# Optimization experiments

Hardware: AMD Instinct MI355X
Metric: run time of the kernel (lower is better)

The kernel has to match this reference:

```python
import jax, jax.numpy as jnp
import numpy as np

# Episode configuration (matches init_kwargs); feature map fixed by module: [64,7,7]
N_WAY, K_SHOT, Q_QUERY, PRJ = 10, 5, 100, 16
DIM, H, W = 64, 7, 7
N_SUP = N_WAY * K_SHOT * PRJ      # 800 support samples
N_QRY = N_WAY * Q_QUERY * PRJ     # 16000 query samples
B = N_SUP + N_QRY                 # 16800
TRIU_I, TRIU_J = np.triu_indices(DIM)  # row-major upper-tri indices, matches torch nonzero order


def setup_inputs() -> dict:
    key = jax.random.key(0)
    k1, k2 = jax.random.split(key)
    feat = jax.random.normal(k1, (B, DIM, H, W), dtype=jnp.float32)
    label = jax.random.randint(k2, (N_QRY,), 0, N_WAY, dtype=jnp.int64)
    # nn.Parameter init: log(1/(2*h*w)) * ones(1,1)
    temp = jnp.log(jnp.ones((1, 1), dtype=jnp.float32) / (2.0 * H * W))
    return {"feat": feat, "temp": temp, "label": label}


def _bdcovpool(x, t):
    # x: [B, dim, h, w] -> Brownian distance covariance matrix [B, dim, dim]
    b, d, h, w = x.shape
    xm = x.reshape(b, d, h * w)
    g = jnp.einsum('bim,bjm->bij', xm, xm)            # x @ x^T, [B,d,d]
    dg = jnp.diagonal(g, axis1=1, axis2=2)            # [B,d]
    # I_M @ (G*I) + (G*I) @ I_M - 2G  ==  diag_j + diag_i - 2G
    dcov = dg[:, None, :] + dg[:, :, None] - 2.0 * g
    dcov = jnp.sqrt(jnp.exp(t) * jnp.clip(dcov, 0.0) + 1e-5)
    # double centering: dcov - rowmean - colmean + totalmean
    rm = jnp.mean(dcov, axis=2, keepdims=True)        # (1/d) dcov @ I_M
    cm = jnp.mean(dcov, axis=1, keepdims=True)        # (1/d) I_M @ dcov
    tm = jnp.mean(dcov, axis=(1, 2), keepdims=True)   # (1/d^2) I_M @ dcov @ I_M
    return dcov - rm - cm + tm


def reference(feat, temp, label):
    v = _bdcovpool(feat, temp)                        # [B, 64, 64]
    tv = v[:, TRIU_I, TRIU_J]                         # Triuvec: [B, 2080]
    support = tv[:N_SUP].reshape(N_WAY, K_SHOT * PRJ, -1).mean(axis=1)  # [n_way, 2080]
    query = tv[N_SUP:]                                # [N_QRY, 2080]
    # negative squared euclidean distance (expanded form of sum((x-y)^2))
    q2 = jnp.sum(query * query, axis=1, keepdims=True)          # [N_QRY,1]
    s2 = jnp.sum(support * support, axis=1)[None, :]             # [1,n_way]
    score = -(q2 + s2 - 2.0 * jnp.einsum('nd,md->nm', query, support))  # [N_QRY, n_way]
    logp = jax.nn.log_softmax(score, axis=-1)
    loss = -jnp.mean(jnp.take_along_axis(logp, label[:, None], axis=1))
    return score, loss
```

## Files before the change

kernel.cpp:

```cpp
#include <hip/hip_runtime.h>
#include <math.h>

#define NWAY   10
#define DIMD   64
#define HWN    49
#define NSUP   800
#define NQRY   16000
#define NTRI   2080
#define FEAT_PER (DIMD*HWN)
#define LDST   68
#define KPAD   72
#define STP    12

typedef __attribute__((ext_vector_type(8))) short bf16x8;
typedef __attribute__((ext_vector_type(4))) float f32x4;

struct __align__(16) BDCShared {
    union {
        float dcov[DIMD*LDST];
        unsigned short hl[2*DIMD*KPAD];
    } u;
    float dg[DIMD];
    float rm[DIMD];
    float w4[4];
    float red[4*12];
};

__device__ __forceinline__ void k2ij(int k, int& io, int& jo) {
    int ii = (int)floorf((129.0f - sqrtf(16641.0f - 8.0f*(float)k)) * 0.5f);
    int off = ii*(129-ii)/2;
    if (off > k) { --ii; off = ii*(129-ii)/2; }
    else {
        int off2 = (ii+1)*(128-ii)/2;
        if (off2 <= k) { ii += 1; off = off2; }
    }
    io = ii;
    jo = ii + (k - off);
}

__device__ __forceinline__ unsigned cvt_pk_bf16(float a, float b) {
    unsigned r;
    asm("v_cvt_pk_bf16_f32 %0, %1, %2" : "=v"(r) : "v"(a), "v"(b));
    return r;
}

__device__ __forceinline__ float bdc_compute(const float* __restrict__ feat,
                                             float et, int sample,
                                             BDCShared& sm) {
    const int tid = threadIdx.x;
    unsigned short* Hh = sm.u.hl;
    unsigned short* Lh = sm.u.hl + DIMD*KPAD;

    {
        const int d = tid & 63, hq = tid >> 6;
        const float* rowp = feat + (size_t)sample * FEAT_PER + d*HWN + hq*16;
        float x[16];
        if (hq < 3) {
            #pragma unroll
            for (int i = 0; i < 16; ++i) x[i] = rowp[i];
        } else {
            x[0] = rowp[0];
            #pragma unroll
            for (int i = 1; i < 16; ++i) x[i] = 0.0f;
        }
        unsigned hp[8], lp[8];
        #pragma unroll
        for (int i = 0; i < 8; ++i) {
            unsigned h = cvt_pk_bf16(x[2*i], x[2*i+1]);
            float h0 = __uint_as_float(h << 16);
            float h1 = __uint_as_float(h & 0xffff0000u);
            hp[i] = h;
            lp[i] = cvt_pk_bf16(x[2*i] - h0, x[2*i+1] - h1);
        }
        uint4* hd = (uint4*)&Hh[d*KPAD + hq*16];
        uint4* ld = (uint4*)&Lh[d*KPAD + hq*16];
        hd[0] = make_uint4(hp[0], hp[1], hp[2], hp[3]);
        hd[1] = make_uint4(hp[4], hp[5], hp[6], hp[7]);
        ld[0] = make_uint4(lp[0], lp[1], lp[2], lp[3]);
        ld[1] = make_uint4(lp[4], lp[5], lp[6], lp[7]);
    }
    __syncthreads();

    const int wv = tid >> 6, lane = tid & 63;
    const int qd = lane >> 4, c15 = lane & 15;
    const int abase = (16*wv + c15)*KPAD + qd*8;
    bf16x8 AH0 = *(const bf16x8*)&Hh[abase];
    bf16x8 AH1 = *(const bf16x8*)&Hh[abase + 32];
    bf16x8 AL0 = *(const bf16x8*)&Lh[abase];
    bf16x8 AL1 = *(const bf16x8*)&Lh[abase + 32];

    f32x4 acc[4];
    #pragma unroll
    for (int J = 0; J < 4; ++J) {
        const int bbase = (16*J + c15)*KPAD + qd*8;
        bf16x8 BH0 = *(const bf16x8*)&Hh[bbase];
        bf16x8 BH1 = *(const bf16x8*)&Hh[bbase + 32];
        bf16x8 BL0 = *(const bf16x8*)&Lh[bbase];
        bf16x8 BL1 = *(const bf16x8*)&Lh[bbase + 32];
        f32x4 a = {0.f, 0.f, 0.f, 0.f};
        a = __builtin_amdgcn_mfma_f32_16x16x32_bf16(AH0, BH0, a, 0, 0, 0);
        a = __builtin_amdgcn_mfma_f32_16x16x32_bf16(AH1, BH1, a, 0, 0, 0);
        a = __builtin_amdgcn_mfma_f32_16x16x32_bf16(AL0, BH0, a, 0, 0, 0);
        a = __builtin_amdgcn_mfma_f32_16x16x32_bf16(AL1, BH1, a, 0, 0, 0);
        a = __builtin_amdgcn_mfma_f32_16x16x32_bf16(AH0, BL0, a, 0, 0, 0);
        a = __builtin_amdgcn_mfma_f32_16x16x32_bf16(AH1, BL1, a, 0, 0, 0);
        acc[J] = a;
    }

    #pragma unroll
    for (int J = 0; J < 4; ++J) {
        if (J == wv) {
            #pragma unroll
            for (int r = 0; r < 4; ++r)
                if (c15 == 4*qd + r) sm.dg[16*wv + c15] = acc[J][r];
        }
    }
    __syncthreads();

    float* dcov = sm.u.dcov;
    f32x4 dgi = *(const f32x4*)&sm.dg[16*wv + 4*qd];
    float rs0 = 0.f, rs1 = 0.f, rs2 = 0.f, rs3 = 0.f;
    #pragma unroll
    for (int J = 0; J < 4; ++J) {
        float dgj = sm.dg[16*J + c15];
        f32x4 o;
        #pragma unroll
        for (int r = 0; r < 4; ++r) {
            float t2 = fmaf(-2.0f, acc[J][r], dgi[r] + dgj);
            t2 = fmaxf(t2, 0.0f);
            o[r] = __builtin_amdgcn_sqrtf(fmaf(et, t2, 1e-5f));
        }
        rs0 += o[0]; rs1 += o[1]; rs2 += o[2]; rs3 += o[3];
        *(f32x4*)&dcov[(16*J + c15)*LDST + 16*wv + 4*qd] = o;
    }
    #pragma unroll
    for (int o = 1; o < 16; o <<= 1) {
        rs0 += __shfl_xor(rs0, o, 64);
        rs1 += __shfl_xor(rs1, o, 64);
        rs2 += __shfl_xor(rs2, o, 64);
        rs3 += __shfl_xor(rs3, o, 64);
    }
    if (c15 == 0) {
        f32x4 rmv = {rs0*(1.0f/64.0f), rs1*(1.0f/64.0f),
                     rs2*(1.0f/64.0f), rs3*(1.0f/64.0f)};
        *(f32x4*)&sm.rm[16*wv + 4*qd] = rmv;
    }
    float tt = (rs0 + rs1) + (rs2 + rs3);
    tt += __shfl_xor(tt, 16, 64);
    tt += __shfl_xor(tt, 32, 64);
    if (lane == 0) sm.w4[wv] = tt;
    __syncthreads();
    return (sm.w4[0] + sm.w4[1] + sm.w4[2] + sm.w4[3]) * (1.0f/4096.0f);
}

__global__ void kern_init(unsigned* __restrict__ table,
                          float* __restrict__ s2,
                          float* __restrict__ loss_slot) {
    int i = blockIdx.x * 256 + threadIdx.x;
    if (i < NTRI) {
        int ii, jj; k2ij(i, ii, jj);
        table[i] = ((unsigned)(ii*LDST + jj) << 16) | ((unsigned)ii << 8) | (unsigned)jj;
    }
    if (i < NWAY) s2[i] = 0.0f;
    if (i == 0) loss_slot[0] = 0.0f;
}

__global__ __launch_bounds__(256, 6) void kern_support(const float* __restrict__ feat,
                                                       const float* __restrict__ temp,
                                                       const unsigned* __restrict__ table,
                                                       float* __restrict__ tvout) {
    __shared__ BDCShared sm;
    float et = __expf(temp[0]);
    int s = blockIdx.x;
    float tm = bdc_compute(feat, et, s, sm);
    float* dst = tvout + (size_t)s * NTRI;
    for (int k = threadIdx.x; k < NTRI; k += 256) {
        unsigned t = table[k];
        dst[k] = sm.u.dcov[t >> 16] - sm.rm[(t >> 8) & 63] - sm.rm[t & 63] + tm;
    }
}

__global__ __launch_bounds__(256) void kern_reduce(const float* __restrict__ tv,
                                                   float* __restrict__ supT,
                                                   float* __restrict__ s2) {
    __shared__ float red[4];
    int m = blockIdx.x / 9, kc = blockIdx.x % 9;
    int k = kc*256 + threadIdx.x;
    float S = 0.0f;
    if (k < NTRI) {
        const float* p = tv + (size_t)(80*m) * NTRI + k;
        float a0 = 0.f, a1 = 0.f, a2 = 0.f, a3 = 0.f;
        for (int s4 = 0; s4 < 80; s4 += 4) {
            a0 += p[(size_t)(s4+0)*NTRI];
            a1 += p[(size_t)(s4+1)*NTRI];
            a2 += p[(size_t)(s4+2)*NTRI];
            a3 += p[(size_t)(s4+3)*NTRI];
        }
        S = ((a0+a1)+(a2+a3)) * (1.0f/80.0f);
        supT[k*STP + m] = S;
    }
    float ps = S * S;
    int lane = threadIdx.x & 63, wv = threadIdx.x >> 6;
    #pragma unroll
    for (int o = 32; o > 0; o >>= 1) ps += __shfl_xor(ps, o, 64);
    if (lane == 0) red[wv] = ps;
    __syncthreads();
    if (threadIdx.x == 0) atomicAdd(&s2[m], red[0]+red[1]+red[2]+red[3]);
}

__global__ __launch_bounds__(256, 6) void kern_query(const float* __restrict__ feat,
                                                     const float* __restrict__ temp,
                                                     const unsigned* __restrict__ table,
                                                     const float* __restrict__ supT,
                                                     const float* __restrict__ s2,
                                                     float* __restrict__ out) {
    __shared__ BDCShared sm;
    float et = __expf(temp[0]);
    int qn = blockIdx.x;
    float tm = bdc_compute(feat, et, NSUP + qn, sm);

    float qq = 0.0f;
    float cr[NWAY];
    #pragma unroll
    for (int m = 0; m < NWAY; ++m) cr[m] = 0.0f;

    for (int k = threadIdx.x; k < NTRI; k += 256) {
        unsigned t = table[k];
        float v = sm.u.dcov[t >> 16] - sm.rm[(t >> 8) & 63] - sm.rm[t & 63] + tm;
        qq = fmaf(v, v, qq);
        const float4* sp = (const float4*)(supT + (size_t)k * STP);
        float4 sa = sp[0], sb = sp[1], sc = sp[2];
        cr[0] = fmaf(v, sa.x, cr[0]);
        cr[1] = fmaf(v, sa.y, cr[1]);
        cr[2] = fmaf(v, sa.z, cr[2]);
        cr[3] = fmaf(v, sa.w, cr[3]);
        cr[4] = fmaf(v, sb.x, cr[4]);
        cr[5] = fmaf(v, sb.y, cr[5]);
        cr[6] = fmaf(v, sb.z, cr[6]);
        cr[7] = fmaf(v, sb.w, cr[7]);
        cr[8] = fmaf(v, sc.x, cr[8]);
        cr[9] = fmaf(v, sc.y, cr[9]);
    }

    int lane = threadIdx.x & 63, wv = threadIdx.x >> 6;
    #pragma unroll
    for (int m = 0; m < NWAY; ++m) {
        float v = cr[m];
        #pragma unroll
        for (int o = 32; o > 0; o >>= 1) v += __shfl_xor(v, o, 64);
        cr[m] = v;
    }
    #pragma unroll
    for (int o = 32; o > 0; o >>= 1) qq += __shfl_xor(qq, o, 64);
    if (lane == 0) {
        #pragma unroll
        for (int m = 0; m < NWAY; ++m) sm.red[wv*12 + m] = cr[m];
        sm.red[wv*12 + 10] = qq;
    }
    __syncthreads();
    if (threadIdx.x < NWAY) {
        int m = threadIdx.x;
        float CR = sm.red[m] + sm.red[12+m] + sm.red[24+m] + sm.red[36+m];
        float QQ = sm.red[10] + sm.red[22] + sm.red[34] + sm.red[46];
        out[(size_t)qn * NWAY + m] = -(QQ + s2[m] - 2.0f*CR);
    }
}

__global__ __launch_bounds__(256) void kern_loss(const float* __restrict__ score,
                                                 const int* __restrict__ label,
                                                 float* __restrict__ loss_out) {
    __shared__ float red[4];
    int n = blockIdx.x * 256 + threadIdx.x;
    float lsum = 0.0f;
    if (n < NQRY) {
        const float* srow = score + (size_t)n * NWAY;
        float s[NWAY];
        float mx = -1e30f;
        #pragma unroll
        for (int m = 0; m < NWAY; ++m) { s[m] = srow[m]; mx = fmaxf(mx, s[m]); }
        float se = 0.0f;
        #pragma unroll
        for (int m = 0; m < NWAY; ++m) se += __expf(s[m] - mx);
        float lse = mx + __logf(se);
        lsum = lse - s[label[n]];
    }
    int lane = threadIdx.x & 63, wv = threadIdx.x >> 6;
    #pragma unroll
    for (int o = 32; o > 0; o >>= 1) lsum += __shfl_xor(lsum, o, 64);
    if (lane == 0) red[wv] = lsum;
    __syncthreads();
    if (threadIdx.x == 0)
        atomicAdd(loss_out, (red[0] + red[1] + red[2] + red[3]) * (1.0f / (float)NQRY));
}

extern "C" void kernel_launch(void* const* d_in, const int* in_sizes, int n_in,
                              void* d_out, int out_size, void* d_ws, size_t ws_size,
                              hipStream_t stream) {
    const float* feat = (const float*)d_in[0];
    const float* temp = (const float*)d_in[1];
    const int*   label = (const int*)d_in[2];
    float* out = (float*)d_out;

    float*    tv    = (float*)d_ws;
    float*    supT  = tv + (size_t)NSUP * NTRI;
    float*    s2    = supT + NTRI*STP;
    unsigned* table = (unsigned*)(s2 + 16);
    float* loss_slot = out + (size_t)NQRY * NWAY;

    kern_init<<<(NTRI + 255)/256, 256, 0, stream>>>(table, s2, loss_slot);
    kern_support<<<NSUP, 256, 0, stream>>>(feat, temp, table, tv);
    kern_reduce<<<NWAY*9, 256, 0, stream>>>(tv, supT, s2);
    kern_query<<<NQRY, 256, 0, stream>>>(feat, temp, table, supT, s2, out);
    kern_loss<<<(NQRY + 255)/256, 256, 0, stream>>>(out, label, loss_slot);
}
```

Before: 346.6 us.

## Keep dcov in registers and score queries against symmetric full support matrices

```diff
diff --git a/kernel.cpp b/kernel.cpp
--- a/kernel.cpp
+++ b/kernel.cpp
@@ -8,22 +8,20 @@
 #define NQRY   16000
 #define NTRI   2080
 #define FEAT_PER (DIMD*HWN)
-#define LDST   68
 #define KPAD   72
-#define STP    12
 
 typedef __attribute__((ext_vector_type(8))) short bf16x8;
 typedef __attribute__((ext_vector_type(4))) float f32x4;
 
 struct __align__(16) BDCShared {
     union {
-        float dcov[DIMD*LDST];
         unsigned short hl[2*DIMD*KPAD];
+        float part[256*12];
     } u;
     float dg[DIMD];
     float rm[DIMD];
     float w4[4];
-    float red[4*12];
+    float red[16];
 };
 
 __device__ __forceinline__ void k2ij(int k, int& io, int& jo) {
@@ -46,7 +44,7 @@
 
 __device__ __forceinline__ float bdc_compute(const float* __restrict__ feat,
                                              float et, int sample,
-                                             BDCShared& sm) {
+                                             BDCShared& sm, f32x4* o, f32x4& rmi) {
     const int tid = threadIdx.x;
     unsigned short* Hh = sm.u.hl;
     unsigned short* Lh = sm.u.hl + DIMD*KPAD;
@@ -117,28 +115,25 @@
     }
     __syncthreads();
 
-    float* dcov = sm.u.dcov;
     f32x4 dgi = *(const f32x4*)&sm.dg[16*wv + 4*qd];
     float rs0 = 0.f, rs1 = 0.f, rs2 = 0.f, rs3 = 0.f;
     #pragma unroll
     for (int J = 0; J < 4; ++J) {
         float dgj = sm.dg[16*J + c15];
-        f32x4 o;
         #pragma unroll
         for (int r = 0; r < 4; ++r) {
             float t2 = fmaf(-2.0f, acc[J][r], dgi[r] + dgj);
             t2 = fmaxf(t2, 0.0f);
-            o[r] = __builtin_amdgcn_sqrtf(fmaf(et, t2, 1e-5f));
-        }
-        rs0 += o[0]; rs1 += o[1]; rs2 += o[2]; rs3 += o[3];
-        *(f32x4*)&dcov[(16*J + c15)*LDST + 16*wv + 4*qd] = o;
-    }
-    #pragma unroll
-    for (int o = 1; o < 16; o <<= 1) {
-        rs0 += __shfl_xor(rs0, o, 64);
-        rs1 += __shfl_xor(rs1, o, 64);
-        rs2 += __shfl_xor(rs2, o, 64);
-        rs3 += __shfl_xor(rs3, o, 64);
+            o[J][r] = __builtin_amdgcn_sqrtf(fmaf(et, t2, 1e-5f));
+        }
+        rs0 += o[J][0]; rs1 += o[J][1]; rs2 += o[J][2]; rs3 += o[J][3];
+    }
+    #pragma unroll
+    for (int off = 1; off < 16; off <<= 1) {
+        rs0 += __shfl_xor(rs0, off, 64);
+        rs1 += __shfl_xor(rs1, off, 64);
+        rs2 += __shfl_xor(rs2, off, 64);
+        rs3 += __shfl_xor(rs3, off, 64);
     }
     if (c15 == 0) {
         f32x4 rmv = {rs0*(1.0f/64.0f), rs1*(1.0f/64.0f),
@@ -150,6 +145,10 @@
     tt += __shfl_xor(tt, 32, 64);
     if (lane == 0) sm.w4[wv] = tt;
     __syncthreads();
+    rmi[0] = rs0 * (1.0f/64.0f);
+    rmi[1] = rs1 * (1.0f/64.0f);
+    rmi[2] = rs2 * (1.0f/64.0f);
+    rmi[3] = rs3 * (1.0f/64.0f);
     return (sm.w4[0] + sm.w4[1] + sm.w4[2] + sm.w4[3]) * (1.0f/4096.0f);
 }
 
@@ -159,7 +158,7 @@
     int i = blockIdx.x * 256 + threadIdx.x;
     if (i < NTRI) {
         int ii, jj; k2ij(i, ii, jj);
-        table[i] = ((unsigned)(ii*LDST + jj) << 16) | ((unsigned)ii << 8) | (unsigned)jj;
+        table[i] = ((unsigned)ii << 8) | (unsigned)jj;
     }
     if (i < NWAY) s2[i] = 0.0f;
     if (i == 0) loss_slot[0] = 0.0f;
@@ -167,26 +166,41 @@
 
 __global__ __launch_bounds__(256, 6) void kern_support(const float* __restrict__ feat,
                                                        const float* __restrict__ temp,
-                                                       const unsigned* __restrict__ table,
                                                        float* __restrict__ tvout) {
     __shared__ BDCShared sm;
     float et = __expf(temp[0]);
     int s = blockIdx.x;
-    float tm = bdc_compute(feat, et, s, sm);
+    f32x4 o[4]; f32x4 rmi;
+    float tm = bdc_compute(feat, et, s, sm, o, rmi);
+
+    const int tid = threadIdx.x;
+    const int wv = tid >> 6, lane = tid & 63;
+    const int qd = lane >> 4, c15 = lane & 15;
+    const int iB = 16*wv + 4*qd;
     float* dst = tvout + (size_t)s * NTRI;
-    for (int k = threadIdx.x; k < NTRI; k += 256) {
-        unsigned t = table[k];
-        dst[k] = sm.u.dcov[t >> 16] - sm.rm[(t >> 8) & 63] - sm.rm[t & 63] + tm;
+    #pragma unroll
+    for (int J = 0; J < 4; ++J) {
+        int j = 16*J + c15;
+        float rmj = sm.rm[j];
+        #pragma unroll
+        for (int r = 0; r < 4; ++r) {
+            int i = iB + r;
+            if (j >= i) {
+                float v = o[J][r] - rmi[r] - rmj + tm;
+                dst[i*(129 - i)/2 + (j - i)] = v;
+            }
+        }
     }
 }
 
 __global__ __launch_bounds__(256) void kern_reduce(const float* __restrict__ tv,
-                                                   float* __restrict__ supT,
+                                                   const unsigned* __restrict__ table,
+                                                   float* __restrict__ Sfull,
                                                    float* __restrict__ s2) {
     __shared__ float red[4];
     int m = blockIdx.x / 9, kc = blockIdx.x % 9;
     int k = kc*256 + threadIdx.x;
-    float S = 0.0f;
+    float ps = 0.0f;
     if (k < NTRI) {
         const float* p = tv + (size_t)(80*m) * NTRI + k;
         float a0 = 0.f, a1 = 0.f, a2 = 0.f, a3 = 0.f;
@@ -196,13 +210,17 @@
             a2 += p[(size_t)(s4+2)*NTRI];
             a3 += p[(size_t)(s4+3)*NTRI];
         }
-        S = ((a0+a1)+(a2+a3)) * (1.0f/80.0f);
-        supT[k*STP + m] = S;
-    }
-    float ps = S * S;
+        float S = ((a0+a1)+(a2+a3)) * (1.0f/80.0f);
+        unsigned t = table[k];
+        int ii = (int)(t >> 8), jj = (int)(t & 255u);
+        float* Sm = Sfull + (size_t)m * 4096;
+        Sm[ii*64 + jj] = S;
+        Sm[jj*64 + ii] = S;
+        ps = S * S;
+    }
     int lane = threadIdx.x & 63, wv = threadIdx.x >> 6;
     #pragma unroll
-    for (int o = 32; o > 0; o >>= 1) ps += __shfl_xor(ps, o, 64);
+    for (int off = 32; off > 0; off >>= 1) ps += __shfl_xor(ps, off, 64);
     if (lane == 0) red[wv] = ps;
     __syncthreads();
     if (threadIdx.x == 0) atomicAdd(&s2[m], red[0]+red[1]+red[2]+red[3]);
@@ -210,60 +228,82 @@
 
 __global__ __launch_bounds__(256, 6) void kern_query(const float* __restrict__ feat,
                                                      const float* __restrict__ temp,
-                                                     const unsigned* __restrict__ table,
-                                                     const float* __restrict__ supT,
+                                                     const float* __restrict__ Sfull,
                                                      const float* __restrict__ s2,
                                                      float* __restrict__ out) {
     __shared__ BDCShared sm;
     float et = __expf(temp[0]);
     int qn = blockIdx.x;
-    float tm = bdc_compute(feat, et, NSUP + qn, sm);
-
-    float qq = 0.0f;
+    f32x4 o[4]; f32x4 rmi;
+    float tm = bdc_compute(feat, et, NSUP + qn, sm, o, rmi);
+
+    const int tid = threadIdx.x;
+    const int wv = tid >> 6, lane = tid & 63;
+    const int qd = lane >> 4, c15 = lane & 15;
+    const int iB = 16*wv + 4*qd;
+
+    f32x4 u[4];
+    #pragma unroll
+    for (int J = 0; J < 4; ++J) {
+        float rmj = sm.rm[16*J + c15];
+        #pragma unroll
+        for (int r = 0; r < 4; ++r) {
+            float v = o[J][r] - rmi[r] - rmj + tm;
+            u[J][r] = 0.5f * v;
+        }
+    }
+    float dadj = 0.0f;
+    if ((c15 >> 2) == qd) {
+        int r0 = c15 & 3;
+        float ud = u[wv][r0] * 2.0f;
+        u[wv][r0] = ud;
+        dadj = ud * ud;
+    }
+    float qq2 = 0.0f;
+    #pragma unroll
+    for (int J = 0; J < 4; ++J) {
+        #pragma unroll
+        for (int r = 0; r < 4; ++r) qq2 = fmaf(u[J][r], u[J][r], qq2);
+    }
+    float qq = 2.0f*qq2 - dadj;
+
     float cr[NWAY];
     #pragma unroll
     for (int m = 0; m < NWAY; ++m) cr[m] = 0.0f;
-
-    for (int k = threadIdx.x; k < NTRI; k += 256) {
-        unsigned t = table[k];
-        float v = sm.u.dcov[t >> 16] - sm.rm[(t >> 8) & 63] - sm.rm[t & 63] + tm;
-        qq = fmaf(v, v, qq);
-        const float4* sp = (const float4*)(supT + (size_t)k * STP);
-        float4 sa = sp[0], sb = sp[1], sc = sp[2];
-        cr[0] = fmaf(v, sa.x, cr[0]);
-        cr[1] = fmaf(v, sa.y, cr[1]);
-        cr[2] = fmaf(v, sa.z, cr[2]);
-        cr[3] = fmaf(v, sa.w, cr[3]);
-        cr[4] = fmaf(v, sb.x, cr[4]);
-        cr[5] = fmaf(v, sb.y, cr[5]);
-        cr[6] = fmaf(v, sb.z, cr[6]);
-        cr[7] = fmaf(v, sb.w, cr[7]);
-        cr[8] = fmaf(v, sc.x, cr[8]);
-        cr[9] = fmaf(v, sc.y, cr[9]);
-    }
-
-    int lane = threadIdx.x & 63, wv = threadIdx.x >> 6;
-    #pragma unroll
-    for (int m = 0; m < NWAY; ++m) {
-        float v = cr[m];
-        #pragma unroll
-        for (int o = 32; o > 0; o >>= 1) v += __shfl_xor(v, o, 64);
-        cr[m] = v;
-    }
-    #pragma unroll
-    for (int o = 32; o > 0; o >>= 1) qq += __shfl_xor(qq, o, 64);
-    if (lane == 0) {
-        #pragma unroll
-        for (int m = 0; m < NWAY; ++m) sm.red[wv*12 + m] = cr[m];
-        sm.red[wv*12 + 10] = qq;
-    }
-    __syncthreads();
-    if (threadIdx.x < NWAY) {
-        int m = threadIdx.x;
-        float CR = sm.red[m] + sm.red[12+m] + sm.red[24+m] + sm.red[36+m];
-        float QQ = sm.red[10] + sm.red[22] + sm.red[34] + sm.red[46];
-        out[(size_t)qn * NWAY + m] = -(QQ + s2[m] - 2.0f*CR);
-    }
+    #pragma unroll
+    for (int J = 0; J < 4; ++J) {
+        const float* sp = Sfull + (16*J + c15)*64 + iB;
+        f32x4 uj = u[J];
+        #pragma unroll
+        for (int m = 0; m < NWAY; ++m) {
+            f32x4 sf = *(const f32x4*)(sp + (size_t)m*4096);
+            cr[m] = fmaf(uj[0], sf[0], cr[m]);
+            cr[m] = fmaf(uj[1], sf[1], cr[m]);
+            cr[m] = fmaf(uj[2], sf[2], cr[m]);
+            cr[m] = fmaf(uj[3], sf[3], cr[m]);
+        }
+    }
+
+    float* part = sm.u.part;
+    f32x4 p0 = {cr[0], cr[1], cr[2], cr[3]};
+    f32x4 p1 = {cr[4], cr[5], cr[6], cr[7]};
+    f32x4 p2 = {cr[8], cr[9], qq, 0.0f};
+    *(f32x4*)&part[tid*12 + 0] = p0;
+    *(f32x4*)&part[tid*12 + 4] = p1;
+    *(f32x4*)&part[tid*12 + 8] = p2;
+    __syncthreads();
+    if (tid < 176) {
+        int m = tid >> 4, g = tid & 15;
+        float s = 0.0f;
+        #pragma unroll
+        for (int t = 0; t < 16; ++t) s += part[(g + 16*t)*12 + m];
+        #pragma unroll
+        for (int off = 1; off < 16; off <<= 1) s += __shfl_xor(s, off, 64);
+        if (g == 0) sm.red[m] = s;
+    }
+    __syncthreads();
+    if (tid < NWAY)
+        out[(size_t)qn * NWAY + tid] = -(sm.red[10] + s2[tid] - 2.0f*sm.red[tid]);
 }
 
 __global__ __launch_bounds__(256) void kern_loss(const float* __restrict__ score,
@@ -286,7 +326,7 @@
     }
     int lane = threadIdx.x & 63, wv = threadIdx.x >> 6;
     #pragma unroll
-    for (int o = 32; o > 0; o >>= 1) lsum += __shfl_xor(lsum, o, 64);
+    for (int off = 32; off > 0; off >>= 1) lsum += __shfl_xor(lsum, off, 64);
     if (lane == 0) red[wv] = lsum;
     __syncthreads();
     if (threadIdx.x == 0)
@@ -296,20 +336,21 @@
 extern "C" void kernel_launch(void* const* d_in, const int* in_sizes, int n_in,
                               void* d_out, int out_size, void* d_ws, size_t ws_size,
                               hipStream_t stream) {
+    (void)in_sizes; (void)n_in; (void)out_size; (void)ws_size;
     const float* feat = (const float*)d_in[0];
     const float* temp = (const float*)d_in[1];
     const int*   label = (const int*)d_in[2];
     float* out = (float*)d_out;
 
     float*    tv    = (float*)d_ws;
-    float*    supT  = tv + (size_t)NSUP * NTRI;
-    float*    s2    = supT + NTRI*STP;
+    float*    Sfull = tv + (size_t)NSUP * NTRI;
+    float*    s2    = Sfull + (size_t)NWAY * 4096;
     unsigned* table = (unsigned*)(s2 + 16);
     float* loss_slot = out + (size_t)NQRY * NWAY;
 
     kern_init<<<(NTRI + 255)/256, 256, 0, stream>>>(table, s2, loss_slot);
-    kern_support<<<NSUP, 256, 0, stream>>>(feat, temp, table, tv);
-    kern_reduce<<<NWAY*9, 256, 0, stream>>>(tv, supT, s2);
-    kern_query<<<NQRY, 256, 0, stream>>>(feat, temp, table, supT, s2, out);
+    kern_support<<<NSUP, 256, 0, stream>>>(feat, temp, tv);
+    kern_reduce<<<NWAY*9, 256, 0, stream>>>(tv, table, Sfull, s2);
+    kern_query<<<NQRY, 256, 0, stream>>>(feat, temp, Sfull, s2, out);
     kern_loss<<<(NQRY + 255)/256, 256, 0, stream>>>(out, label, loss_slot);
 }
```

Measured after the change: 683.1 us. 1.97x slower.

## Apply double centering in registers and write support triu directly from accumulators

Applied to the files above, without the earlier changes.

```diff
diff --git a/kernel.cpp b/kernel.cpp
--- a/kernel.cpp
+++ b/kernel.cpp
@@ -17,13 +17,14 @@
 
 struct __align__(16) BDCShared {
     union {
+        unsigned short hl[2*DIMD*KPAD];
         float dcov[DIMD*LDST];
-        unsigned short hl[2*DIMD*KPAD];
+        float part[256*12];
     } u;
     float dg[DIMD];
     float rm[DIMD];
     float w4[4];
-    float red[4*12];
+    float red[16];
 };
 
 __device__ __forceinline__ void k2ij(int k, int& io, int& jo) {
@@ -45,8 +46,9 @@
 }
 
 __device__ __forceinline__ float bdc_compute(const float* __restrict__ feat,
-                                             float et, int sample,
-                                             BDCShared& sm) {
+                                             float et, int sample, BDCShared& sm,
+                                             f32x4& v0, f32x4& v1, f32x4& v2,
+                                             f32x4& v3) {
     const int tid = threadIdx.x;
     unsigned short* Hh = sm.u.hl;
     unsigned short* Lh = sm.u.hl + DIMD*KPAD;
@@ -117,28 +119,29 @@
     }
     __syncthreads();
 
-    float* dcov = sm.u.dcov;
     f32x4 dgi = *(const f32x4*)&sm.dg[16*wv + 4*qd];
     float rs0 = 0.f, rs1 = 0.f, rs2 = 0.f, rs3 = 0.f;
-    #pragma unroll
-    for (int J = 0; J < 4; ++J) {
-        float dgj = sm.dg[16*J + c15];
-        f32x4 o;
-        #pragma unroll
-        for (int r = 0; r < 4; ++r) {
-            float t2 = fmaf(-2.0f, acc[J][r], dgi[r] + dgj);
-            t2 = fmaxf(t2, 0.0f);
-            o[r] = __builtin_amdgcn_sqrtf(fmaf(et, t2, 1e-5f));
-        }
-        rs0 += o[0]; rs1 += o[1]; rs2 += o[2]; rs3 += o[3];
-        *(f32x4*)&dcov[(16*J + c15)*LDST + 16*wv + 4*qd] = o;
-    }
-    #pragma unroll
-    for (int o = 1; o < 16; o <<= 1) {
-        rs0 += __shfl_xor(rs0, o, 64);
-        rs1 += __shfl_xor(rs1, o, 64);
-        rs2 += __shfl_xor(rs2, o, 64);
-        rs3 += __shfl_xor(rs3, o, 64);
+#define DCOV_J(J, VJ)                                                          \
+    {   float dgj = sm.dg[16*(J) + c15];                                       \
+        _Pragma("unroll")                                                      \
+        for (int r = 0; r < 4; ++r) {                                          \
+            float t2 = fmaf(-2.0f, acc[J][r], dgi[r] + dgj);                   \
+            t2 = fmaxf(t2, 0.0f);                                              \
+            VJ[r] = __builtin_amdgcn_sqrtf(fmaf(et, t2, 1e-5f));               \
+        }                                                                      \
+        rs0 += VJ[0]; rs1 += VJ[1]; rs2 += VJ[2]; rs3 += VJ[3]; }
+    DCOV_J(0, v0)
+    DCOV_J(1, v1)
+    DCOV_J(2, v2)
+    DCOV_J(3, v3)
+#undef DCOV_J
+
+    #pragma unroll
+    for (int off = 1; off < 16; off <<= 1) {
+        rs0 += __shfl_xor(rs0, off, 64);
+        rs1 += __shfl_xor(rs1, off, 64);
+        rs2 += __shfl_xor(rs2, off, 64);
+        rs3 += __shfl_xor(rs3, off, 64);
     }
     if (c15 == 0) {
         f32x4 rmv = {rs0*(1.0f/64.0f), rs1*(1.0f/64.0f),
@@ -150,7 +153,26 @@
     tt += __shfl_xor(tt, 32, 64);
     if (lane == 0) sm.w4[wv] = tt;
     __syncthreads();
-    return (sm.w4[0] + sm.w4[1] + sm.w4[2] + sm.w4[3]) * (1.0f/4096.0f);
+    float tm = (sm.w4[0] + sm.w4[1] + sm.w4[2] + sm.w4[3]) * (1.0f/4096.0f);
+
+    const float rmi0 = rs0*(1.0f/64.0f), rmi1 = rs1*(1.0f/64.0f),
+                rmi2 = rs2*(1.0f/64.0f), rmi3 = rs3*(1.0f/64.0f);
+    float* dcov = sm.u.dcov;
+    const int iB = 16*wv + 4*qd;
+#define CENTER_J(J, VJ)                                                        \
+    {   float rmj = sm.rm[16*(J) + c15] - tm;                                  \
+        VJ[0] = VJ[0] - rmi0 - rmj;                                            \
+        VJ[1] = VJ[1] - rmi1 - rmj;                                            \
+        VJ[2] = VJ[2] - rmi2 - rmj;                                            \
+        VJ[3] = VJ[3] - rmi3 - rmj;                                            \
+        *(f32x4*)&dcov[(16*(J) + c15)*LDST + iB] = VJ; }
+    CENTER_J(0, v0)
+    CENTER_J(1, v1)
+    CENTER_J(2, v2)
+    CENTER_J(3, v3)
+#undef CENTER_J
+    __syncthreads();
+    return tm;
 }
 
 __global__ void kern_init(unsigned* __restrict__ table,
@@ -167,20 +189,33 @@
 
 __global__ __launch_bounds__(256, 6) void kern_support(const float* __restrict__ feat,
                                                        const float* __restrict__ temp,
-                                                       const unsigned* __restrict__ table,
                                                        float* __restrict__ tvout) {
     __shared__ BDCShared sm;
     float et = __expf(temp[0]);
     int s = blockIdx.x;
-    float tm = bdc_compute(feat, et, s, sm);
+    f32x4 v0, v1, v2, v3;
+    bdc_compute(feat, et, s, sm, v0, v1, v2, v3);
+
+    const int tid = threadIdx.x;
+    const int wv = tid >> 6, lane = tid & 63;
+    const int qd = lane >> 4, c15 = lane & 15;
+    const int iB = 16*wv + 4*qd;
     float* dst = tvout + (size_t)s * NTRI;
-    for (int k = threadIdx.x; k < NTRI; k += 256) {
-        unsigned t = table[k];
-        dst[k] = sm.u.dcov[t >> 16] - sm.rm[(t >> 8) & 63] - sm.rm[t & 63] + tm;
-    }
+#define SUP_J(J, VJ)                                                           \
+    {   int j = 16*(J) + c15;                                                  \
+        _Pragma("unroll")                                                      \
+        for (int r = 0; r < 4; ++r) {                                          \
+            int i = iB + r;                                                    \
+            if (j >= i) dst[i*(129 - i)/2 + (j - i)] = VJ[r]; } }
+    SUP_J(0, v0)
+    SUP_J(1, v1)
+    SUP_J(2, v2)
+    SUP_J(3, v3)
+#undef SUP_J
 }
 
 __global__ __launch_bounds__(256) void kern_reduce(const float* __restrict__ tv,
+                                                   const unsigned* __restrict__ table,
                                                    float* __restrict__ supT,
                                                    float* __restrict__ s2) {
     __shared__ float red[4];
@@ -202,7 +237,7 @@
     float ps = S * S;
     int lane = threadIdx.x & 63, wv = threadIdx.x >> 6;
     #pragma unroll
-    for (int o = 32; o > 0; o >>= 1) ps += __shfl_xor(ps, o, 64);
+    for (int off = 32; off > 0; off >>= 1) ps += __shfl_xor(ps, off, 64);
     if (lane == 0) red[wv] = ps;
     __syncthreads();
     if (threadIdx.x == 0) atomicAdd(&s2[m], red[0]+red[1]+red[2]+red[3]);
@@ -217,16 +252,19 @@
     __shared__ BDCShared sm;
     float et = __expf(temp[0]);
     int qn = blockIdx.x;
-    float tm = bdc_compute(feat, et, NSUP + qn, sm);
-
+    f32x4 v0, v1, v2, v3;
+    bdc_compute(feat, et, NSUP + qn, sm, v0, v1, v2, v3);
+
+    const int tid = threadIdx.x;
     float qq = 0.0f;
     float cr[NWAY];
     #pragma unroll
     for (int m = 0; m < NWAY; ++m) cr[m] = 0.0f;
 
-    for (int k = threadIdx.x; k < NTRI; k += 256) {
+    const float* dcov = sm.u.dcov;
+    for (int k = tid; k < NTRI; k += 256) {
         unsigned t = table[k];
-        float v = sm.u.dcov[t >> 16] - sm.rm[(t >> 8) & 63] - sm.rm[t & 63] + tm;
+        float v = dcov[t >> 16];
         qq = fmaf(v, v, qq);
         const float4* sp = (const float4*)(supT + (size_t)k * STP);
         float4 sa = sp[0], sb = sp[1], sc = sp[2];
@@ -241,29 +279,28 @@
         cr[8] = fmaf(v, sc.x, cr[8]);
         cr[9] = fmaf(v, sc.y, cr[9]);
     }
-
-    int lane = threadIdx.x & 63, wv = threadIdx.x >> 6;
-    #pragma unroll
-    for (int m = 0; m < NWAY; ++m) {
-        float v = cr[m];
-        #pragma unroll
-        for (int o = 32; o > 0; o >>= 1) v += __shfl_xor(v, o, 64);
-        cr[m] = v;
-    }
-    #pragma unroll
-    for (int o = 32; o > 0; o >>= 1) qq += __shfl_xor(qq, o, 64);
-    if (lane == 0) {
-        #pragma unroll
-        for (int m = 0; m < NWAY; ++m) sm.red[wv*12 + m] = cr[m];
-        sm.red[wv*12 + 10] = qq;
-    }
-    __syncthreads();
-    if (threadIdx.x < NWAY) {
-        int m = threadIdx.x;
-        float CR = sm.red[m] + sm.red[12+m] + sm.red[24+m] + sm.red[36+m];
-        float QQ = sm.red[10] + sm.red[22] + sm.red[34] + sm.red[46];
-        out[(size_t)qn * NWAY + m] = -(QQ + s2[m] - 2.0f*CR);
-    }
+    __syncthreads();
+
+    float* part = sm.u.part;
+    f32x4 p0 = {cr[0], cr[1], cr[2], cr[3]};
+    f32x4 p1 = {cr[4], cr[5], cr[6], cr[7]};
+    f32x4 p2 = {cr[8], cr[9], qq, 0.0f};
+    *(f32x4*)&part[tid*12 + 0] = p0;
+    *(f32x4*)&part[tid*12 + 4] = p1;
+    *(f32x4*)&part[tid*12 + 8] = p2;
+    __syncthreads();
+    if (tid < 176) {
+        int m = tid >> 4, g = tid & 15;
+        float s = 0.0f;
+        #pragma unroll
+        for (int t = 0; t < 16; ++t) s += part[(g + 16*t)*12 + m];
+        #pragma unroll
+        for (int off = 1; off < 16; off <<= 1) s += __shfl_xor(s, off, 64);
+        if (g == 0) sm.red[m] = s;
+    }
+    __syncthreads();
+    if (tid < NWAY)
+        out[(size_t)qn * NWAY + tid] = -(sm.red[10] + s2[tid] - 2.0f*sm.red[tid]);
 }
 
 __global__ __launch_bounds__(256) void kern_loss(const float* __restrict__ score,
@@ -286,7 +323,7 @@
     }
     int lane = threadIdx.x & 63, wv = threadIdx.x >> 6;
     #pragma unroll
-    for (int o = 32; o > 0; o >>= 1) lsum += __shfl_xor(lsum, o, 64);
+    for (int off = 32; off > 0; off >>= 1) lsum += __shfl_xor(lsum, off, 64);
     if (lane == 0) red[wv] = lsum;
     __syncthreads();
     if (threadIdx.x == 0)
@@ -296,6 +333,7 @@
 extern "C" void kernel_launch(void* const* d_in, const int* in_sizes, int n_in,
                               void* d_out, int out_size, void* d_ws, size_t ws_size,
                               hipStream_t stream) {
+    (void)in_sizes; (void)n_in; (void)out_size; (void)ws_size;
     const float* feat = (const float*)d_in[0];
     const float* temp = (const float*)d_in[1];
     const int*   label = (const int*)d_in[2];
@@ -308,8 +346,8 @@
     float* loss_slot = out + (size_t)NQRY * NWAY;
 
     kern_init<<<(NTRI + 255)/256, 256, 0, stream>>>(table, s2, loss_slot);
-    kern_support<<<NSUP, 256, 0, stream>>>(feat, temp, table, tv);
-    kern_reduce<<<NWAY*9, 256, 0, stream>>>(tv, supT, s2);
+    kern_support<<<NSUP, 256, 0, stream>>>(feat, temp, tv);
+    kern_reduce<<<NWAY*9, 256, 0, stream>>>(tv, table, supT, s2);
     kern_query<<<NQRY, 256, 0, stream>>>(feat, temp, table, supT, s2, out);
     kern_loss<<<(NQRY + 255)/256, 256, 0, stream>>>(out, label, loss_slot);
 }
```

New measurement: 350.0 us. About the same (+1.0%).
